# Kernel tuning notes

Hardware: AMD Instinct MI355X
Metric: run time of the kernel (lower is better)

Reference implementation:

```python
import jax, jax.numpy as jnp
import numpy as np

N_NODES = 100000


def _gcn_layer(x, W, b, src, dst, n):
    # h = x @ W  (small feature dims)
    h = x @ W
    # add self-loops (GCNConv default: add_self_loops=True, weight 1)
    loop = jnp.arange(n, dtype=src.dtype)
    s = jnp.concatenate([src, loop])
    d = jnp.concatenate([dst, loop])
    # symmetric degree normalization: deg over incoming edges (incl. self-loops)
    deg = jax.ops.segment_sum(jnp.ones_like(d, dtype=h.dtype), d, num_segments=n)
    dinv = jnp.where(deg > 0, jax.lax.rsqrt(deg), 0.0)
    norm = dinv[s] * dinv[d]  # [E+N]
    msg = h[s] * norm[:, None]  # gather + scale
    out = jax.ops.segment_sum(msg, d, num_segments=n)  # scatter-add aggregation
    return out + b


def setup_inputs() -> dict:
    key = jax.random.key(0)
    k1, k2, k3, k4 = jax.random.split(key, 4)
    x = jax.random.normal(k1, (N_NODES, 512), dtype=jnp.float32)
    edge_index = jax.random.randint(k2, (2, 3200000), 0, N_NODES, dtype=jnp.int32)
    W1 = jax.random.normal(k3, (512, 16), dtype=jnp.float32) * (1.0 / np.sqrt(512))
    b1 = jnp.zeros((16,), dtype=jnp.float32)
    W2 = jax.random.normal(k4, (16, 40), dtype=jnp.float32) * (1.0 / np.sqrt(16))
    b2 = jnp.zeros((40,), dtype=jnp.float32)
    return {"x": x, "edge_index": edge_index, "W1": W1, "b1": b1, "W2": W2, "b2": b2}


def reference(x, edge_index, W1, b1, W2, b2):
    n = x.shape[0]
    src, dst = edge_index[0], edge_index[1]
    h = jax.nn.relu(_gcn_layer(x, W1, b1, src, dst, n))
    # F.dropout(training=False) is identity in eval mode
    h = _gcn_layer(h, W2, b2, src, dst, n)
    return jax.nn.log_softmax(h, axis=1)
```

## Files before the change

kernel.cpp:

```cpp
#include <hip/hip_runtime.h>
#include <hip/hip_fp16.h>


#define NFEAT_IN 512
#define NF1 16
#define NF2 40
#define BK_LG 8
#define TILE 8192
#define XSTR 264
#define WSTR 520

typedef _Float16 f16x8 __attribute__((ext_vector_type(8)));
typedef _Float16 f16x4 __attribute__((ext_vector_type(4)));
typedef float f32x4 __attribute__((ext_vector_type(4)));

__global__ void k_bhist(const int* __restrict__ dst, int* __restrict__ gbsz, int E, int nbk) {
  __shared__ int h[512];
  for (int i = threadIdx.x; i < nbk; i += 256) h[i] = 0;
  __syncthreads();
  int stride = gridDim.x * 256;
  for (int e = blockIdx.x * 256 + threadIdx.x; e < E; e += stride)
    atomicAdd(&h[dst[e] >> BK_LG], 1);
  __syncthreads();
  for (int i = threadIdx.x; i < nbk; i += 256)
    if (h[i]) atomicAdd(&gbsz[i], h[i]);
}

__global__ void k_scanb(const int* __restrict__ gbsz, int* __restrict__ boff,
                        int* __restrict__ gcur, int* __restrict__ rp,
                        int nbk, int n, int E) {
  __shared__ int s[512];
  int t = threadIdx.x;
  s[t] = (t < nbk) ? gbsz[t] : 0;
  __syncthreads();
  for (int o = 1; o < 512; o <<= 1) {
    int v = (t >= o) ? s[t - o] : 0;
    __syncthreads();
    s[t] += v;
    __syncthreads();
  }
  if (t < nbk) {
    int ex = s[t] - gbsz[t];
    boff[t] = ex;
    gcur[t] = ex;
  }
  if (t == 0) { boff[nbk] = E; rp[n] = E; }
}

__global__ void k_part(const int* __restrict__ src, const int* __restrict__ dst,
                       int* __restrict__ gcur, unsigned int* __restrict__ ebuf,
                       int E, int nbk) {
  __shared__ int hist[512];
  __shared__ int hbase[512];
  int chunk = (E + gridDim.x - 1) / gridDim.x;
  int beg = blockIdx.x * chunk;
  int end = min(E, beg + chunk);
  for (int t0 = beg; t0 < end; t0 += TILE) {
    int t1 = min(end, t0 + TILE);
    for (int i = threadIdx.x; i < nbk; i += 256) hist[i] = 0;
    __syncthreads();
    for (int i = t0 + threadIdx.x; i < t1; i += 256)
      atomicAdd(&hist[dst[i] >> BK_LG], 1);
    __syncthreads();
    for (int i = threadIdx.x; i < nbk; i += 256) {
      int c = hist[i];
      hbase[i] = c ? atomicAdd(&gcur[i], c) : 0;
      hist[i] = 0;
    }
    __syncthreads();
    for (int i = t0 + threadIdx.x; i < t1; i += 256) {
      int d = dst[i];
      int b = d >> BK_LG;
      int r = atomicAdd(&hist[b], 1);
      ebuf[hbase[b] + r] = ((unsigned)(d & ((1 << BK_LG) - 1)) << 17) | (unsigned)src[i];
    }
    __syncthreads();
  }
}

__global__ __launch_bounds__(256) void k_sortb(
    const unsigned int* __restrict__ ebuf, const int* __restrict__ boff,
    int* __restrict__ esrc, int* __restrict__ rp, float* __restrict__ dinv,
    int n) {
  __shared__ int hist[256];
  __shared__ int scan[256];
  __shared__ int cur[256];
  int b = blockIdx.x;
  int e0 = boff[b], e1 = boff[b + 1];
  hist[threadIdx.x] = 0;
  __syncthreads();
  for (int e = e0 + threadIdx.x; e < e1; e += 256)
    atomicAdd(&hist[ebuf[e] >> 17], 1);
  __syncthreads();
  scan[threadIdx.x] = hist[threadIdx.x];
  __syncthreads();
  for (int o = 1; o < 256; o <<= 1) {
    int v = (threadIdx.x >= o) ? scan[threadIdx.x - o] : 0;
    __syncthreads();
    scan[threadIdx.x] += v;
    __syncthreads();
  }
  int excl = scan[threadIdx.x] - hist[threadIdx.x];
  cur[threadIdx.x] = e0 + excl;
  int vg = (b << BK_LG) + threadIdx.x;
  if (vg < n) {
    rp[vg] = e0 + excl;
    dinv[vg] = rsqrtf((float)(hist[threadIdx.x] + 1));
  }
  __syncthreads();
  for (int e = e0 + threadIdx.x; e < e1; e += 256) {
    unsigned p = ebuf[e];
    int pos = atomicAdd(&cur[p >> 17], 1);
    esrc[pos] = (int)(p & 0x1FFFF);
  }
}

__global__ __launch_bounds__(256) void k_gemm1(
    const float* __restrict__ x, const float* __restrict__ W1,
    const float* __restrict__ dinv, __half* __restrict__ h1s, int ntiles) {
  __shared__ _Float16 Wt[NF1 * WSTR];
  __shared__ _Float16 xs[4][16 * XSTR];
  for (int i = threadIdx.x; i < NFEAT_IN * NF1; i += 256) {
    int k = i >> 4, f = i & 15;
    Wt[f * WSTR + k] = (_Float16)W1[i];
  }
  __syncthreads();

  int w = threadIdx.x >> 6;
  int l = threadIdx.x & 63;
  int tile = blockIdx.x * 4 + w;
  if (tile >= ntiles) return;
  int v0 = tile << 4;

  int fr = l & 15;
  int kb = l >> 4;
  _Float16* xsw = &xs[w][0];
  const _Float16* xrow = &xsw[fr * XSTR + (kb << 3)];
  const _Float16* wrow = &Wt[fr * WSTR + (kb << 3)];

  f32x4 acc = {0.f, 0.f, 0.f, 0.f};
#pragma unroll
  for (int half = 0; half < 2; ++half) {
#pragma unroll
    for (int i = 0; i < 16; ++i) {
      float4 a = *(const float4*)&x[(size_t)(v0 + i) * NFEAT_IN + half * 256 + l * 4];
      f16x4 hv = {(_Float16)a.x, (_Float16)a.y, (_Float16)a.z, (_Float16)a.w};
      *(f16x4*)&xsw[i * XSTR + l * 4] = hv;
    }
#pragma unroll
    for (int kk = 0; kk < 8; ++kk) {
      f16x8 av = *(const f16x8*)&xrow[kk * 32];
      f16x8 bv = *(const f16x8*)&wrow[half * 256 + kk * 32];
      acc = __builtin_amdgcn_mfma_f32_16x16x32_f16(av, bv, acc, 0, 0, 0);
    }
  }
  int rbase = kb << 2;
#pragma unroll
  for (int q = 0; q < 4; ++q) {
    int v = v0 + rbase + q;
    h1s[(size_t)v * NF1 + fr] = __float2half(acc[q] * dinv[v]);
  }
}

__global__ __launch_bounds__(256) void k_agg1(
    const int* __restrict__ rp, const int* __restrict__ esrc,
    const __half* __restrict__ h, const float* __restrict__ dinv,
    const float* __restrict__ b1, __half* __restrict__ as2) {
  int t = blockIdx.x * 256 + threadIdx.x;
  int v = t >> 4, f = t & 15;
  int beg = rp[v], end = rp[v + 1];
  float sum = __half2float(h[t]);
  int e = beg;
  for (; e + 8 <= end; e += 8) {
    int s0 = esrc[e],     s1 = esrc[e + 1], s2 = esrc[e + 2], s3 = esrc[e + 3];
    int s4 = esrc[e + 4], s5 = esrc[e + 5], s6 = esrc[e + 6], s7 = esrc[e + 7];
    float a0 = __half2float(h[(size_t)s0 * NF1 + f]);
    float a1 = __half2float(h[(size_t)s1 * NF1 + f]);
    float a2 = __half2float(h[(size_t)s2 * NF1 + f]);
    float a3 = __half2float(h[(size_t)s3 * NF1 + f]);
    float a4 = __half2float(h[(size_t)s4 * NF1 + f]);
    float a5 = __half2float(h[(size_t)s5 * NF1 + f]);
    float a6 = __half2float(h[(size_t)s6 * NF1 + f]);
    float a7 = __half2float(h[(size_t)s7 * NF1 + f]);
    sum += ((a0 + a1) + (a2 + a3)) + ((a4 + a5) + (a6 + a7));
  }
  for (; e < end; ++e) sum += __half2float(h[(size_t)esrc[e] * NF1 + f]);
  float dv = dinv[v];
  float a = fmaf(dv, sum, b1[f]);
  as2[t] = __float2half((a > 0.f ? a : 0.f) * dv);
}

__global__ __launch_bounds__(256) void k_agg2fin(
    const int* __restrict__ rp, const int* __restrict__ esrc,
    const __half* __restrict__ h, const float* __restrict__ dinv,
    const float* __restrict__ W2, const float* __restrict__ b2,
    float* __restrict__ out) {
  __shared__ float W2s[NF1 * NF2];
  __shared__ float b2s[NF2];
  __shared__ float sa[256];
  for (int i = threadIdx.x; i < NF1 * NF2; i += 256) W2s[i] = W2[i];
  if (threadIdx.x < NF2) b2s[threadIdx.x] = b2[threadIdx.x];
  int t = blockIdx.x * 256 + threadIdx.x;
  int v = t >> 4, f = t & 15;
  int beg = rp[v], end = rp[v + 1];
  float sum = __half2float(h[t]);
  int e = beg;
  for (; e + 8 <= end; e += 8) {
    int s0 = esrc[e],     s1 = esrc[e + 1], s2 = esrc[e + 2], s3 = esrc[e + 3];
    int s4 = esrc[e + 4], s5 = esrc[e + 5], s6 = esrc[e + 6], s7 = esrc[e + 7];
    float a0 = __half2float(h[(size_t)s0 * NF1 + f]);
    float a1 = __half2float(h[(size_t)s1 * NF1 + f]);
    float a2 = __half2float(h[(size_t)s2 * NF1 + f]);
    float a3 = __half2float(h[(size_t)s3 * NF1 + f]);
    float a4 = __half2float(h[(size_t)s4 * NF1 + f]);
    float a5 = __half2float(h[(size_t)s5 * NF1 + f]);
    float a6 = __half2float(h[(size_t)s6 * NF1 + f]);
    float a7 = __half2float(h[(size_t)s7 * NF1 + f]);
    sum += ((a0 + a1) + (a2 + a3)) + ((a4 + a5) + (a6 + a7));
  }
  for (; e < end; ++e) sum += __half2float(h[(size_t)esrc[e] * NF1 + f]);
  sa[threadIdx.x] = dinv[v] * sum;
  __syncthreads();
  const float* av = &sa[(threadIdx.x >> 4) << 4];
  float z0 = b2s[f], z1 = b2s[f + 16], z2 = (f < 8) ? b2s[f + 32] : -1e30f;
#pragma unroll
  for (int ff = 0; ff < NF1; ++ff) {
    float a = av[ff];
    z0 = fmaf(a, W2s[ff * NF2 + f], z0);
    z1 = fmaf(a, W2s[ff * NF2 + f + 16], z1);
    if (f < 8) z2 = fmaf(a, W2s[ff * NF2 + f + 32], z2);
  }
  float m = fmaxf(fmaxf(z0, z1), z2);
#pragma unroll
  for (int o = 8; o > 0; o >>= 1) m = fmaxf(m, __shfl_xor(m, o, 16));
  float s = __expf(z0 - m) + __expf(z1 - m) + ((f < 8) ? __expf(z2 - m) : 0.f);
#pragma unroll
  for (int o = 8; o > 0; o >>= 1) s += __shfl_xor(s, o, 16);
  float ls = m + __logf(s);
  float* orow = out + (size_t)v * NF2;
  orow[f] = z0 - ls;
  orow[f + 16] = z1 - ls;
  if (f < 8) orow[f + 32] = z2 - ls;
}

extern "C" void kernel_launch(void* const* d_in, const int* in_sizes, int n_in,
                              void* d_out, int out_size, void* d_ws, size_t ws_size,
                              hipStream_t stream) {
  const float* x  = (const float*)d_in[0];
  const int*   ei = (const int*)d_in[1];
  const float* W1 = (const float*)d_in[2];
  const float* b1 = (const float*)d_in[3];
  const float* W2 = (const float*)d_in[4];
  const float* b2 = (const float*)d_in[5];
  int n = in_sizes[0] / NFEAT_IN;
  int E = in_sizes[1] / 2;
  const int* src = ei;
  const int* dst = ei + E;
  float* out = (float*)d_out;
  int nbk = ((n - 1) >> BK_LG) + 1;
  int ntiles = n >> 4;

  char* ws = (char*)d_ws;
  size_t off = 0;
  auto alloc = [&](size_t bytes) { size_t o = off; off = (off + bytes + 63) & ~63ULL; return o; };
  int*   gbsz = (int*)(ws + alloc(512 * 4));
  int*   boff = (int*)(ws + alloc(513 * 4));
  int*   gcur = (int*)(ws + alloc(512 * 4));
  int*   rp   = (int*)(ws + alloc((size_t)(n + 1) * 4));
  float* dinv = (float*)(ws + alloc((size_t)n * 4));
  unsigned int* ebuf = (unsigned int*)(ws + alloc((size_t)E * 4));
  int*   esrc = (int*)(ws + alloc((size_t)E * 4));
  __half* h1s = (__half*)(ws + alloc((size_t)n * NF1 * 2));
  __half* as2 = (__half*)(ws + alloc((size_t)n * NF1 * 2));

  hipMemsetAsync(gbsz, 0, 512 * 4, stream);

  k_bhist<<<1024, 256, 0, stream>>>(dst, gbsz, E, nbk);
  k_scanb<<<1, 512, 0, stream>>>(gbsz, boff, gcur, rp, nbk, n, E);
  k_part <<<256, 256, 0, stream>>>(src, dst, gcur, ebuf, E, nbk);
  k_sortb<<<nbk, 256, 0, stream>>>(ebuf, boff, esrc, rp, dinv, n);
  k_gemm1<<<(ntiles + 3) / 4, 256, 0, stream>>>(x, W1, dinv, h1s, ntiles);
  k_agg1 <<<((size_t)n * NF1) / 256, 256, 0, stream>>>(rp, esrc, h1s, dinv, b1, as2);
  k_agg2fin<<<((size_t)n * NF1) / 256, 256, 0, stream>>>(rp, esrc, as2, dinv, W2, b2, out);
}
```

Measured before the change: 488.7 us.

## Vectorize aggregation to 16-byte row gathers and widen partition/sort launches

The two aggregation kernels now assign two threads per node, each gathering a 16-byte half of the fp16 feature row, so each edge costs one wide load per thread instead of sixteen 2-byte loads spread across threads. The fused layer-2 kernel computes 20 output logits per thread, reduces the softmax across the two-thread pair, and writes float4 stores. The per-bucket sort uses 1024-thread blocks, and the partition kernel uses a smaller tile with 4x more blocks for more parallelism. The trade-off is higher register use per thread and fewer independent threads hiding gather latency.

```diff
diff --git a/kernel.cpp b/kernel.cpp
--- a/kernel.cpp
+++ b/kernel.cpp
@@ -6,7 +6,7 @@
 #define NF1 16
 #define NF2 40
 #define BK_LG 8
-#define TILE 8192
+#define TILE 4096
 #define XSTR 264
 #define WSTR 520
 
@@ -78,7 +78,7 @@
   }
 }
 
-__global__ __launch_bounds__(256) void k_sortb(
+__global__ __launch_bounds__(1024) void k_sortb(
     const unsigned int* __restrict__ ebuf, const int* __restrict__ boff,
     int* __restrict__ esrc, int* __restrict__ rp, float* __restrict__ dinv,
     int n) {
@@ -86,29 +86,32 @@
   __shared__ int scan[256];
   __shared__ int cur[256];
   int b = blockIdx.x;
+  int tid = threadIdx.x;
   int e0 = boff[b], e1 = boff[b + 1];
-  hist[threadIdx.x] = 0;
-  __syncthreads();
-  for (int e = e0 + threadIdx.x; e < e1; e += 256)
+  if (tid < 256) hist[tid] = 0;
+  __syncthreads();
+  for (int e = e0 + tid; e < e1; e += 1024)
     atomicAdd(&hist[ebuf[e] >> 17], 1);
   __syncthreads();
-  scan[threadIdx.x] = hist[threadIdx.x];
+  if (tid < 256) scan[tid] = hist[tid];
   __syncthreads();
   for (int o = 1; o < 256; o <<= 1) {
-    int v = (threadIdx.x >= o) ? scan[threadIdx.x - o] : 0;
-    __syncthreads();
-    scan[threadIdx.x] += v;
-    __syncthreads();
-  }
-  int excl = scan[threadIdx.x] - hist[threadIdx.x];
-  cur[threadIdx.x] = e0 + excl;
-  int vg = (b << BK_LG) + threadIdx.x;
-  if (vg < n) {
-    rp[vg] = e0 + excl;
-    dinv[vg] = rsqrtf((float)(hist[threadIdx.x] + 1));
-  }
-  __syncthreads();
-  for (int e = e0 + threadIdx.x; e < e1; e += 256) {
+    int v = (tid < 256 && tid >= o) ? scan[tid - o] : 0;
+    __syncthreads();
+    if (tid < 256) scan[tid] += v;
+    __syncthreads();
+  }
+  if (tid < 256) {
+    int excl = scan[tid] - hist[tid];
+    cur[tid] = e0 + excl;
+    int vg = (b << BK_LG) + tid;
+    if (vg < n) {
+      rp[vg] = e0 + excl;
+      dinv[vg] = rsqrtf((float)(hist[tid] + 1));
+    }
+  }
+  __syncthreads();
+  for (int e = e0 + tid; e < e1; e += 1024) {
     unsigned p = ebuf[e];
     int pos = atomicAdd(&cur[p >> 17], 1);
     esrc[pos] = (int)(p & 0x1FFFF);
@@ -125,19 +128,16 @@
     Wt[f * WSTR + k] = (_Float16)W1[i];
   }
   __syncthreads();
-
   int w = threadIdx.x >> 6;
   int l = threadIdx.x & 63;
   int tile = blockIdx.x * 4 + w;
   if (tile >= ntiles) return;
   int v0 = tile << 4;
-
   int fr = l & 15;
   int kb = l >> 4;
   _Float16* xsw = &xs[w][0];
   const _Float16* xrow = &xsw[fr * XSTR + (kb << 3)];
   const _Float16* wrow = &Wt[fr * WSTR + (kb << 3)];
-
   f32x4 acc = {0.f, 0.f, 0.f, 0.f};
 #pragma unroll
   for (int half = 0; half < 2; ++half) {
@@ -165,82 +165,111 @@
 __global__ __launch_bounds__(256) void k_agg1(
     const int* __restrict__ rp, const int* __restrict__ esrc,
     const __half* __restrict__ h, const float* __restrict__ dinv,
-    const float* __restrict__ b1, __half* __restrict__ as2) {
+    const float* __restrict__ b1, __half* __restrict__ as2, int n2) {
   int t = blockIdx.x * 256 + threadIdx.x;
-  int v = t >> 4, f = t & 15;
+  if (t >= n2) return;
+  int v = t >> 1, hw = t & 1;
   int beg = rp[v], end = rp[v + 1];
-  float sum = __half2float(h[t]);
+  const f16x8* hp = (const f16x8*)h;
+  f16x8 sv = hp[(size_t)v * 2 + hw];
+  float sum[8];
+#pragma unroll
+  for (int j = 0; j < 8; ++j) sum[j] = (float)sv[j];
   int e = beg;
-  for (; e + 8 <= end; e += 8) {
-    int s0 = esrc[e],     s1 = esrc[e + 1], s2 = esrc[e + 2], s3 = esrc[e + 3];
-    int s4 = esrc[e + 4], s5 = esrc[e + 5], s6 = esrc[e + 6], s7 = esrc[e + 7];
-    float a0 = __half2float(h[(size_t)s0 * NF1 + f]);
-    float a1 = __half2float(h[(size_t)s1 * NF1 + f]);
-    float a2 = __half2float(h[(size_t)s2 * NF1 + f]);
-    float a3 = __half2float(h[(size_t)s3 * NF1 + f]);
-    float a4 = __half2float(h[(size_t)s4 * NF1 + f]);
-    float a5 = __half2float(h[(size_t)s5 * NF1 + f]);
-    float a6 = __half2float(h[(size_t)s6 * NF1 + f]);
-    float a7 = __half2float(h[(size_t)s7 * NF1 + f]);
-    sum += ((a0 + a1) + (a2 + a3)) + ((a4 + a5) + (a6 + a7));
-  }
-  for (; e < end; ++e) sum += __half2float(h[(size_t)esrc[e] * NF1 + f]);
+  for (; e + 4 <= end; e += 4) {
+    int s0 = esrc[e], s1 = esrc[e + 1], s2 = esrc[e + 2], s3 = esrc[e + 3];
+    f16x8 r0 = hp[(size_t)s0 * 2 + hw];
+    f16x8 r1 = hp[(size_t)s1 * 2 + hw];
+    f16x8 r2 = hp[(size_t)s2 * 2 + hw];
+    f16x8 r3 = hp[(size_t)s3 * 2 + hw];
+#pragma unroll
+    for (int j = 0; j < 8; ++j)
+      sum[j] += ((float)r0[j] + (float)r1[j]) + ((float)r2[j] + (float)r3[j]);
+  }
+  for (; e < end; ++e) {
+    f16x8 r = hp[(size_t)esrc[e] * 2 + hw];
+#pragma unroll
+    for (int j = 0; j < 8; ++j) sum[j] += (float)r[j];
+  }
   float dv = dinv[v];
-  float a = fmaf(dv, sum, b1[f]);
-  as2[t] = __float2half((a > 0.f ? a : 0.f) * dv);
-}
-
+  const float4* b1p = (const float4*)b1;
+  float4 bA = b1p[hw * 2], bB = b1p[hw * 2 + 1];
+  float bb[8] = {bA.x, bA.y, bA.z, bA.w, bB.x, bB.y, bB.z, bB.w};
+  f16x8 o;
+#pragma unroll
+  for (int j = 0; j < 8; ++j) {
+    float a = fmaf(dv, sum[j], bb[j]);
+    o[j] = (_Float16)((a > 0.f ? a : 0.f) * dv);
+  }
+  ((f16x8*)as2)[(size_t)v * 2 + hw] = o;
+}
+
+#define SASTR 17
 __global__ __launch_bounds__(256) void k_agg2fin(
     const int* __restrict__ rp, const int* __restrict__ esrc,
     const __half* __restrict__ h, const float* __restrict__ dinv,
     const float* __restrict__ W2, const float* __restrict__ b2,
-    float* __restrict__ out) {
+    float* __restrict__ out, int n2) {
   __shared__ float W2s[NF1 * NF2];
   __shared__ float b2s[NF2];
-  __shared__ float sa[256];
+  __shared__ float sa[128 * SASTR];
   for (int i = threadIdx.x; i < NF1 * NF2; i += 256) W2s[i] = W2[i];
   if (threadIdx.x < NF2) b2s[threadIdx.x] = b2[threadIdx.x];
   int t = blockIdx.x * 256 + threadIdx.x;
-  int v = t >> 4, f = t & 15;
-  int beg = rp[v], end = rp[v + 1];
-  float sum = __half2float(h[t]);
-  int e = beg;
-  for (; e + 8 <= end; e += 8) {
-    int s0 = esrc[e],     s1 = esrc[e + 1], s2 = esrc[e + 2], s3 = esrc[e + 3];
-    int s4 = esrc[e + 4], s5 = esrc[e + 5], s6 = esrc[e + 6], s7 = esrc[e + 7];
-    float a0 = __half2float(h[(size_t)s0 * NF1 + f]);
-    float a1 = __half2float(h[(size_t)s1 * NF1 + f]);
-    float a2 = __half2float(h[(size_t)s2 * NF1 + f]);
-    float a3 = __half2float(h[(size_t)s3 * NF1 + f]);
-    float a4 = __half2float(h[(size_t)s4 * NF1 + f]);
-    float a5 = __half2float(h[(size_t)s5 * NF1 + f]);
-    float a6 = __half2float(h[(size_t)s6 * NF1 + f]);
-    float a7 = __half2float(h[(size_t)s7 * NF1 + f]);
-    sum += ((a0 + a1) + (a2 + a3)) + ((a4 + a5) + (a6 + a7));
-  }
-  for (; e < end; ++e) sum += __half2float(h[(size_t)esrc[e] * NF1 + f]);
-  sa[threadIdx.x] = dinv[v] * sum;
-  __syncthreads();
-  const float* av = &sa[(threadIdx.x >> 4) << 4];
-  float z0 = b2s[f], z1 = b2s[f + 16], z2 = (f < 8) ? b2s[f + 32] : -1e30f;
-#pragma unroll
-  for (int ff = 0; ff < NF1; ++ff) {
-    float a = av[ff];
-    z0 = fmaf(a, W2s[ff * NF2 + f], z0);
-    z1 = fmaf(a, W2s[ff * NF2 + f + 16], z1);
-    if (f < 8) z2 = fmaf(a, W2s[ff * NF2 + f + 32], z2);
-  }
-  float m = fmaxf(fmaxf(z0, z1), z2);
-#pragma unroll
-  for (int o = 8; o > 0; o >>= 1) m = fmaxf(m, __shfl_xor(m, o, 16));
-  float s = __expf(z0 - m) + __expf(z1 - m) + ((f < 8) ? __expf(z2 - m) : 0.f);
-#pragma unroll
-  for (int o = 8; o > 0; o >>= 1) s += __shfl_xor(s, o, 16);
+  int v = t >> 1, hw = t & 1, nl = threadIdx.x >> 1;
+  bool valid = t < n2;
+  if (valid) {
+    int beg = rp[v], end = rp[v + 1];
+    const f16x8* hp = (const f16x8*)h;
+    f16x8 sv = hp[(size_t)v * 2 + hw];
+    float sum[8];
+#pragma unroll
+    for (int j = 0; j < 8; ++j) sum[j] = (float)sv[j];
+    int e = beg;
+    for (; e + 4 <= end; e += 4) {
+      int s0 = esrc[e], s1 = esrc[e + 1], s2 = esrc[e + 2], s3 = esrc[e + 3];
+      f16x8 r0 = hp[(size_t)s0 * 2 + hw];
+      f16x8 r1 = hp[(size_t)s1 * 2 + hw];
+      f16x8 r2 = hp[(size_t)s2 * 2 + hw];
+      f16x8 r3 = hp[(size_t)s3 * 2 + hw];
+#pragma unroll
+      for (int j = 0; j < 8; ++j)
+        sum[j] += ((float)r0[j] + (float)r1[j]) + ((float)r2[j] + (float)r3[j]);
+    }
+    for (; e < end; ++e) {
+      f16x8 r = hp[(size_t)esrc[e] * 2 + hw];
+#pragma unroll
+      for (int j = 0; j < 8; ++j) sum[j] += (float)r[j];
+    }
+    float dv = dinv[v];
+#pragma unroll
+    for (int j = 0; j < 8; ++j) sa[nl * SASTR + hw * 8 + j] = dv * sum[j];
+  }
+  __syncthreads();
+  if (!valid) return;
+  const float* av = &sa[nl * SASTR];
+  float z[20];
+  float m = -1e30f;
+#pragma unroll
+  for (int j = 0; j < 20; ++j) {
+    int g = hw * 20 + j;
+    float acc = b2s[g];
+#pragma unroll
+    for (int ff = 0; ff < NF1; ++ff) acc = fmaf(av[ff], W2s[ff * NF2 + g], acc);
+    z[j] = acc;
+    m = fmaxf(m, acc);
+  }
+  m = fmaxf(m, __shfl_xor(m, 1, 2));
+  float s = 0.f;
+#pragma unroll
+  for (int j = 0; j < 20; ++j) s += __expf(z[j] - m);
+  s += __shfl_xor(s, 1, 2);
   float ls = m + __logf(s);
-  float* orow = out + (size_t)v * NF2;
-  orow[f] = z0 - ls;
-  orow[f + 16] = z1 - ls;
-  if (f < 8) orow[f + 32] = z2 - ls;
+  float4* orow = (float4*)(out + (size_t)v * NF2 + hw * 20);
+#pragma unroll
+  for (int q = 0; q < 5; ++q)
+    orow[q] = make_float4(z[4 * q] - ls, z[4 * q + 1] - ls,
+                          z[4 * q + 2] - ls, z[4 * q + 3] - ls);
 }
 
 extern "C" void kernel_launch(void* const* d_in, const int* in_sizes, int n_in,
@@ -259,6 +288,7 @@
   float* out = (float*)d_out;
   int nbk = ((n - 1) >> BK_LG) + 1;
   int ntiles = n >> 4;
+  int n2 = n * 2;
 
   char* ws = (char*)d_ws;
   size_t off = 0;
@@ -277,9 +307,9 @@
 
   k_bhist<<<1024, 256, 0, stream>>>(dst, gbsz, E, nbk);
   k_scanb<<<1, 512, 0, stream>>>(gbsz, boff, gcur, rp, nbk, n, E);
-  k_part <<<256, 256, 0, stream>>>(src, dst, gcur, ebuf, E, nbk);
-  k_sortb<<<nbk, 256, 0, stream>>>(ebuf, boff, esrc, rp, dinv, n);
+  k_part <<<1024, 256, 0, stream>>>(src, dst, gcur, ebuf, E, nbk);
+  k_sortb<<<nbk, 1024, 0, stream>>>(ebuf, boff, esrc, rp, dinv, n);
   k_gemm1<<<(ntiles + 3) / 4, 256, 0, stream>>>(x, W1, dinv, h1s, ntiles);
-  k_agg1 <<<((size_t)n * NF1) / 256, 256, 0, stream>>>(rp, esrc, h1s, dinv, b1, as2);
-  k_agg2fin<<<((size_t)n * NF1) / 256, 256, 0, stream>>>(rp, esrc, as2, dinv, W2, b2, out);
-}
+  k_agg1 <<<(n2 + 255) / 256, 256, 0, stream>>>(rp, esrc, h1s, dinv, b1, as2, n2);
+  k_agg2fin<<<(n2 + 255) / 256, 256, 0, stream>>>(rp, esrc, as2, dinv, W2, b2, out, n2);
+}
```

Result: no change. 494.7 us (+1.2%).
